# Optimization experiments

Measured on AMD Instinct MI355X. Metric: run time of the kernel, lower is better.

The kernel has to match this reference:

```python
import jax, jax.numpy as jnp
import numpy as np

B, T, D, DS = 8, 4096, 1024, 64


def setup_inputs() -> dict:
    key = jax.random.key(0)
    ks = jax.random.split(key, 9)
    s = 0.02
    return {
        "x": jax.random.normal(ks[0], (B, T, D), dtype=jnp.float32),
        "Wq": jax.random.normal(ks[1], (DS, D), dtype=jnp.float32) * s,
        "bq": jnp.zeros((DS,), dtype=jnp.float32),
        "Wk": jax.random.normal(ks[2], (DS, D), dtype=jnp.float32) * s,
        "bk": jnp.zeros((DS,), dtype=jnp.float32),
        "Wv": jax.random.normal(ks[3], (DS, D), dtype=jnp.float32) * s,
        "bv": jnp.zeros((DS,), dtype=jnp.float32),
        "decay": jnp.full((DS,), 0.95, dtype=jnp.float32),
        "Wo": jax.random.normal(ks[4], (D, DS), dtype=jnp.float32) * s,
        "bo": jnp.zeros((D,), dtype=jnp.float32),
    }


def reference(x, Wq, bq, Wk, bk, Wv, bv, decay, Wo, bo):
    # projections: [B,T,DS]
    q = jnp.einsum('btd,sd->bts', x, Wq) + bq
    k = jnp.einsum('btd,sd->bts', x, Wk) + bk
    v = jnp.einsum('btd,sd->bts', x, Wv) + bv
    d = jax.nn.sigmoid(decay)  # [DS]

    def step(S, qkv_t):
        q_t, k_t, v_t = qkv_t  # each [B, DS]
        # diag(d) @ S + v k^T  (rank-1 update per batch)
        S = d[None, :, None] * S + v_t[:, :, None] * k_t[:, None, :]
        o = jnp.einsum('bij,bj->bi', S, q_t)
        return S, o

    S0 = jnp.zeros((x.shape[0], d.shape[0], d.shape[0]), dtype=x.dtype)
    qkv = (jnp.swapaxes(q, 0, 1), jnp.swapaxes(k, 0, 1), jnp.swapaxes(v, 0, 1))  # [T,B,DS]
    _, outs = jax.lax.scan(step, S0, qkv)  # outs: [T,B,DS]
    scan_out = jnp.swapaxes(outs, 0, 1)  # [B,T,DS]
    return x + jnp.einsum('bts,ds->btd', scan_out, Wo) + bo
```

## Files before the change

kernel.cpp:

```cpp
#include <hip/hip_runtime.h>
#include <cstdint>
#include <cstddef>
#include <cmath>

#define Bb 8
#define Tt 4096
#define Dd 1024
#define DS 64
#define Mm (Bb*Tt)
#define PAD 68

typedef __bf16 bf16x8 __attribute__((ext_vector_type(8)));
typedef __bf16 bf16x4v __attribute__((ext_vector_type(4)));
typedef float f32x4 __attribute__((ext_vector_type(4)));

__device__ __forceinline__ float4* ldsP(float* buf, int row, int col4) {
  return (float4*)(buf + row * PAD + (((col4) ^ ((row >> 3) & 7)) << 2));
}

__global__ __launch_bounds__(256) void convert_w(
    const float* __restrict__ Wq, const float* __restrict__ Wk,
    const float* __restrict__ Wv, const float* __restrict__ Wo,
    __bf16* __restrict__ Wqkvb, __bf16* __restrict__ Wob)
{
  int idx = blockIdx.x * 256 + threadIdx.x;
  if (idx < 196608) {
    float v = (idx < 65536) ? Wq[idx]
            : (idx < 131072) ? Wk[idx - 65536] : Wv[idx - 131072];
    Wqkvb[idx] = (__bf16)v;
  }
  if (idx < 65536) Wob[idx] = (__bf16)Wo[idx];
}

__global__ __launch_bounds__(256) void qkv_mfma(
    const float* __restrict__ x, const __bf16* __restrict__ Wb,
    const float* __restrict__ bq, const float* __restrict__ bk,
    const float* __restrict__ bv, float* __restrict__ qkv)
{
  __shared__ __bf16 xs[2][64 * 64];

  const int tid = threadIdx.x;
  const int w   = tid >> 6;
  const int l   = tid & 63;
  const int m0  = blockIdx.x * 64;
  const int c0  = w * 48;
  const int lr  = l & 15;
  const int lk  = l >> 4;

  const int sr0 = tid >> 4;
  const int sc4 = tid & 15;
  const float* xsrc = x + (size_t)(m0 + sr0) * 1024 + sc4 * 4;

  f32x4 acc[3][4] = {};

  float4 f[4];
  #pragma unroll
  for (int g = 0; g < 4; ++g)
    f[g] = *(const float4*)(xsrc + (size_t)g * 16 * 1024);
  #pragma unroll
  for (int g = 0; g < 4; ++g) {
    bf16x4v h;
    h[0] = (__bf16)f[g].x; h[1] = (__bf16)f[g].y;
    h[2] = (__bf16)f[g].z; h[3] = (__bf16)f[g].w;
    int row = sr0 + 16 * g;
    *(bf16x4v*)((char*)xs[0] + row * 128 + ((sc4 * 8) ^ ((row & 7) << 4))) = h;
  }

  int cur = 0;
  for (int k0 = 0; k0 < 1024; k0 += 64) {
    const bool hasNext = (k0 + 64 < 1024);
    if (hasNext) {
      #pragma unroll
      for (int g = 0; g < 4; ++g)
        f[g] = *(const float4*)(xsrc + (size_t)g * 16 * 1024 + k0 + 64);
    }

    __syncthreads();

    if (hasNext) {
      #pragma unroll
      for (int g = 0; g < 4; ++g) {
        bf16x4v h;
        h[0] = (__bf16)f[g].x; h[1] = (__bf16)f[g].y;
        h[2] = (__bf16)f[g].z; h[3] = (__bf16)f[g].w;
        int row = sr0 + 16 * g;
        *(bf16x4v*)((char*)xs[cur ^ 1] + row * 128 + ((sc4 * 8) ^ ((row & 7) << 4))) = h;
      }
    }

    #pragma unroll
    for (int ks = 0; ks < 2; ++ks) {
      bf16x8 wf[3], xf[4];
      #pragma unroll
      for (int jf = 0; jf < 3; ++jf)
        wf[jf] = *(const bf16x8*)(Wb + (size_t)(c0 + jf * 16 + lr) * 1024
                                     + k0 + ks * 32 + lk * 8);
      #pragma unroll
      for (int mf = 0; mf < 4; ++mf) {
        int row = mf * 16 + lr;
        int boff = row * 128 + ((ks * 64 + lk * 16) ^ ((row & 7) << 4));
        xf[mf] = *(const bf16x8*)((const char*)xs[cur] + boff);
      }
      #pragma unroll
      for (int jf = 0; jf < 3; ++jf)
        #pragma unroll
        for (int mf = 0; mf < 4; ++mf)
          acc[jf][mf] = __builtin_amdgcn_mfma_f32_16x16x32_bf16(
              wf[jf], xf[mf], acc[jf][mf], 0, 0, 0);
    }
    cur ^= 1;
  }

  #pragma unroll
  for (int jf = 0; jf < 3; ++jf) {
    int j0 = c0 + jf * 16 + lk * 4;
    const float* bsrc = (j0 < 64) ? (bq + j0)
                      : (j0 < 128) ? (bk + j0 - 64) : (bv + j0 - 128);
    float4 b4 = *(const float4*)bsrc;
    #pragma unroll
    for (int mf = 0; mf < 4; ++mf) {
      int m = m0 + mf * 16 + lr;
      float4 o;
      o.x = acc[jf][mf][0] + b4.x;
      o.y = acc[jf][mf][1] + b4.y;
      o.z = acc[jf][mf][2] + b4.z;
      o.w = acc[jf][mf][3] + b4.w;
      *(float4*)(qkv + (size_t)m * 192 + j0) = o;
    }
  }
}

__global__ __launch_bounds__(256) void scan_chunk_a(
    const float* __restrict__ qkv, const float* __restrict__ decay,
    float* __restrict__ Ubuf, float* __restrict__ so)
{
  __shared__ float Qs[64 * PAD];
  __shared__ float Ks[64 * PAD];
  __shared__ float Vs[64 * PAD];
  __shared__ float l2d[64];

  const int tid = threadIdx.x;
  const int bc  = blockIdx.x;
  const int b   = bc >> 6;
  const int ch  = bc & 63;
  const int ti  = tid >> 4;
  const int tj  = tid & 15;

  const float* base = qkv + ((size_t)(b * Tt + ch * 64)) * 192;

  #pragma unroll
  for (int it = 0; it < 12; ++it) {
    int idx = tid + it * 256;
    int row = idx / 48, f = idx % 48;
    float4 g = *(const float4*)(base + (size_t)row * 192 + f * 4);
    float4* dst;
    if (f < 16)      dst = ldsP(Qs, row, f);
    else if (f < 32) dst = ldsP(Ks, row, f - 16);
    else             dst = ldsP(Vs, row, f - 32);
    *dst = g;
  }
  if (tid < 64) {
    float d = 1.0f / (1.0f + expf(-decay[tid]));
    l2d[tid] = log2f(d);
  }
  __syncthreads();

  {
    int s = tid >> 2;
    #pragma unroll
    for (int g4 = 0; g4 < 4; ++g4) {
      int col4 = (tid & 3) * 4 + g4;
      float4* p = ldsP(Vs, s, col4);
      float4 v = *p;
      float e0 = exp2f(-(float)s * l2d[col4 * 4 + 0]);
      float e1 = exp2f(-(float)s * l2d[col4 * 4 + 1]);
      float e2 = exp2f(-(float)s * l2d[col4 * 4 + 2]);
      float e3 = exp2f(-(float)s * l2d[col4 * 4 + 3]);
      v.x *= e0; v.y *= e1; v.z *= e2; v.w *= e3;
      *p = v;
    }
  }

  float gval[4][4] = {};
  #pragma unroll
  for (int kk4 = 0; kk4 < 16; ++kk4) {
    float4 K4[4], Q4[4];
    #pragma unroll
    for (int r = 0; r < 4; ++r) K4[r] = *ldsP(Ks, ti * 4 + r, kk4);
    #pragma unroll
    for (int c = 0; c < 4; ++c) Q4[c] = *ldsP(Qs, tj * 4 + c, kk4);
    #pragma unroll
    for (int r = 0; r < 4; ++r)
      #pragma unroll
      for (int c = 0; c < 4; ++c) {
        gval[r][c] = fmaf(K4[r].x, Q4[c].x, gval[r][c]);
        gval[r][c] = fmaf(K4[r].y, Q4[c].y, gval[r][c]);
        gval[r][c] = fmaf(K4[r].z, Q4[c].z, gval[r][c]);
        gval[r][c] = fmaf(K4[r].w, Q4[c].w, gval[r][c]);
      }
  }
  #pragma unroll
  for (int r = 0; r < 4; ++r)
    #pragma unroll
    for (int c = 0; c < 4; ++c)
      if (ti * 4 + r > tj * 4 + c) gval[r][c] = 0.0f;

  __syncthreads();

  #pragma unroll
  for (int r = 0; r < 4; ++r) {
    float4 g4 = {gval[r][0], gval[r][1], gval[r][2], gval[r][3]};
    *ldsP(Qs, ti * 4 + r, tj) = g4;
  }
  __syncthreads();

  float uacc[4][4] = {};
  float oacc[4][4] = {};
  for (int s = 0; s < 64; ++s) {
    float4 Vti = *ldsP(Vs, s, ti);
    float4 Ktj = *ldsP(Ks, s, tj);
    float4 Gti = *ldsP(Qs, s, ti);
    float4 Vtj = *ldsP(Vs, s, tj);
    const float vi[4] = {Vti.x, Vti.y, Vti.z, Vti.w};
    const float kj[4] = {Ktj.x, Ktj.y, Ktj.z, Ktj.w};
    const float gu[4] = {Gti.x, Gti.y, Gti.z, Gti.w};
    const float vj[4] = {Vtj.x, Vtj.y, Vtj.z, Vtj.w};
    #pragma unroll
    for (int r = 0; r < 4; ++r)
      #pragma unroll
      for (int c = 0; c < 4; ++c) {
        uacc[r][c] = fmaf(vi[r], kj[c], uacc[r][c]);
        oacc[r][c] = fmaf(gu[r], vj[c], oacc[r][c]);
      }
  }

  #pragma unroll
  for (int r = 0; r < 4; ++r) {
    int i = ti * 4 + r;
    float d63 = exp2f(63.0f * l2d[i]);
    float4 o = {uacc[r][0] * d63, uacc[r][1] * d63,
                uacc[r][2] * d63, uacc[r][3] * d63};
    *(float4*)(Ubuf + ((size_t)bc * 64 + i) * 64 + tj * 4) = o;
  }
  #pragma unroll
  for (int r = 0; r < 4; ++r) {
    int u = ti * 4 + r;
    float e0 = exp2f((float)u * l2d[tj * 4 + 0]);
    float e1 = exp2f((float)u * l2d[tj * 4 + 1]);
    float e2 = exp2f((float)u * l2d[tj * 4 + 2]);
    float e3 = exp2f((float)u * l2d[tj * 4 + 3]);
    float4 o = {oacc[r][0] * e0, oacc[r][1] * e1,
                oacc[r][2] * e2, oacc[r][3] * e3};
    *(float4*)(so + ((size_t)(b * Tt + ch * 64 + u)) * 64 + tj * 4) = o;
  }
}

__global__ __launch_bounds__(64) void scan_state(
    const float* __restrict__ decay, float* __restrict__ Ubuf)
{
  const int b  = blockIdx.x >> 4;
  const int jq = blockIdx.x & 15;
  const int i  = threadIdx.x;

  float d = 1.0f / (1.0f + expf(-decay[i]));
  float d2 = d * d, d4 = d2 * d2, d8 = d4 * d4;
  float d16 = d8 * d8, d32 = d16 * d16, d64 = d32 * d32;

  float* base = Ubuf + ((size_t)b * 64) * 4096 + (size_t)i * 64 + jq * 4;

  float4 S = {0.f, 0.f, 0.f, 0.f};
  float4 u0 = *(const float4*)(base + 0 * 4096);
  float4 u1 = *(const float4*)(base + 1 * 4096);
  float4 u2 = *(const float4*)(base + 2 * 4096);
  float4 u3 = *(const float4*)(base + 3 * 4096);

  for (int c = 0; c < 64; c += 4) {
    float4 n0 = u0, n1 = u1, n2 = u2, n3 = u3;
    if (c + 4 < 64) {
      n0 = *(const float4*)(base + (size_t)(c + 4) * 4096);
      n1 = *(const float4*)(base + (size_t)(c + 5) * 4096);
      n2 = *(const float4*)(base + (size_t)(c + 6) * 4096);
      n3 = *(const float4*)(base + (size_t)(c + 7) * 4096);
    }
    *(float4*)(base + (size_t)(c + 0) * 4096) = S;
    S.x = fmaf(d64, S.x, u0.x); S.y = fmaf(d64, S.y, u0.y);
    S.z = fmaf(d64, S.z, u0.z); S.w = fmaf(d64, S.w, u0.w);
    *(float4*)(base + (size_t)(c + 1) * 4096) = S;
    S.x = fmaf(d64, S.x, u1.x); S.y = fmaf(d64, S.y, u1.y);
    S.z = fmaf(d64, S.z, u1.z); S.w = fmaf(d64, S.w, u1.w);
    *(float4*)(base + (size_t)(c + 2) * 4096) = S;
    S.x = fmaf(d64, S.x, u2.x); S.y = fmaf(d64, S.y, u2.y);
    S.z = fmaf(d64, S.z, u2.z); S.w = fmaf(d64, S.w, u2.w);
    *(float4*)(base + (size_t)(c + 3) * 4096) = S;
    S.x = fmaf(d64, S.x, u3.x); S.y = fmaf(d64, S.y, u3.y);
    S.z = fmaf(d64, S.z, u3.z); S.w = fmaf(d64, S.w, u3.w);
    u0 = n0; u1 = n1; u2 = n2; u3 = n3;
  }
}

__global__ __launch_bounds__(256) void scan_chunk_c(
    const float* __restrict__ qkv, const float* __restrict__ decay,
    const float* __restrict__ Sbuf, const float* __restrict__ so,
    __bf16* __restrict__ sob)
{
  __shared__ float Ss[64 * PAD];
  __shared__ float Qs[64 * PAD];
  __shared__ float l2d[64];

  const int tid = threadIdx.x;
  const int bc  = blockIdx.x;
  const int b   = bc >> 6;
  const int ch  = bc & 63;
  const int ti  = tid >> 4;
  const int tj  = tid & 15;

  #pragma unroll
  for (int it = 0; it < 4; ++it) {
    int idx = tid + it * 256;
    int row = idx >> 4, col4 = idx & 15;
    float4 s4 = *(const float4*)(Sbuf + (size_t)bc * 4096 + (size_t)row * 64 + col4 * 4);
    *ldsP(Ss, row, col4) = s4;
    float4 q4 = *(const float4*)(qkv + ((size_t)(b * Tt + ch * 64 + row)) * 192 + col4 * 4);
    *ldsP(Qs, row, col4) = q4;
  }
  if (tid < 64) {
    float d = 1.0f / (1.0f + expf(-decay[tid]));
    l2d[tid] = log2f(d);
  }
  __syncthreads();

  float acc[4][4] = {};
  #pragma unroll
  for (int j4 = 0; j4 < 16; ++j4) {
    float4 Q4[4], S4[4];
    #pragma unroll
    for (int r = 0; r < 4; ++r) Q4[r] = *ldsP(Qs, ti * 4 + r, j4);
    #pragma unroll
    for (int c = 0; c < 4; ++c) S4[c] = *ldsP(Ss, tj * 4 + c, j4);
    #pragma unroll
    for (int r = 0; r < 4; ++r)
      #pragma unroll
      for (int c = 0; c < 4; ++c) {
        acc[r][c] = fmaf(Q4[r].x, S4[c].x, acc[r][c]);
        acc[r][c] = fmaf(Q4[r].y, S4[c].y, acc[r][c]);
        acc[r][c] = fmaf(Q4[r].z, S4[c].z, acc[r][c]);
        acc[r][c] = fmaf(Q4[r].w, S4[c].w, acc[r][c]);
      }
  }

  #pragma unroll
  for (int r = 0; r < 4; ++r) {
    int u = ti * 4 + r;
    size_t row = (size_t)(b * Tt + ch * 64 + u);
    float4 prev = *(const float4*)(so + row * 64 + tj * 4);
    float e0 = exp2f((float)(u + 1) * l2d[tj * 4 + 0]);
    float e1 = exp2f((float)(u + 1) * l2d[tj * 4 + 1]);
    float e2 = exp2f((float)(u + 1) * l2d[tj * 4 + 2]);
    float e3 = exp2f((float)(u + 1) * l2d[tj * 4 + 3]);
    bf16x4v ov;
    ov[0] = (__bf16)fmaf(acc[r][0], e0, prev.x);
    ov[1] = (__bf16)fmaf(acc[r][1], e1, prev.y);
    ov[2] = (__bf16)fmaf(acc[r][2], e2, prev.z);
    ov[3] = (__bf16)fmaf(acc[r][3], e3, prev.w);
    *(bf16x4v*)(sob + row * 64 + tj * 4) = ov;
  }
}

__global__ __launch_bounds__(256) void out_mfma(
    const float* __restrict__ x, const __bf16* __restrict__ sob,
    const __bf16* __restrict__ Wob, const float* __restrict__ bo,
    float* __restrict__ out)
{
  __shared__ float ps[4][16 * 64];

  const int bid = blockIdx.x;
  const int rb  = bid >> 2;
  const int jq  = bid & 3;
  const int w   = threadIdx.x >> 6;
  const int l   = threadIdx.x & 63;
  const int lr  = l & 15;
  const int lk  = l >> 4;
  const int m0  = rb * 64 + w * 16;
  const int er  = l >> 4;
  const int ec  = l & 15;

  const __bf16* bp = sob + (size_t)(m0 + lr) * 64 + lk * 8;
  bf16x8 bf0 = *(const bf16x8*)(bp);
  bf16x8 bf1 = *(const bf16x8*)(bp + 32);

  float* myps = ps[w];

  #pragma unroll
  for (int jj = 0; jj < 4; ++jj) {
    const int j0 = (jq * 4 + jj) * 64;

    float4 xv[4];
    #pragma unroll
    for (int k = 0; k < 4; ++k)
      xv[k] = *(const float4*)(x + (size_t)(m0 + er + 4 * k) * 1024 + j0 + ec * 4);
    float4 b4 = *(const float4*)(bo + j0 + ec * 4);

    const __bf16* ap = Wob + (size_t)(j0 + lr) * 64 + lk * 8;
    f32x4 acc[4];
    #pragma unroll
    for (int jf = 0; jf < 4; ++jf) {
      bf16x8 a0 = *(const bf16x8*)(ap + (size_t)jf * 16 * 64);
      bf16x8 a1 = *(const bf16x8*)(ap + (size_t)jf * 16 * 64 + 32);
      f32x4 t = {0.f, 0.f, 0.f, 0.f};
      t = __builtin_amdgcn_mfma_f32_16x16x32_bf16(a0, bf0, t, 0, 0, 0);
      t = __builtin_amdgcn_mfma_f32_16x16x32_bf16(a1, bf1, t, 0, 0, 0);
      acc[jf] = t;
    }

    #pragma unroll
    for (int jf = 0; jf < 4; ++jf) {
      int c4 = jf * 4 + lk;
      float4 v = {acc[jf][0], acc[jf][1], acc[jf][2], acc[jf][3]};
      *(float4*)((char*)myps + lr * 256 + ((c4 * 16) ^ ((lr & 7) << 4))) = v;
    }

    #pragma unroll
    for (int k = 0; k < 4; ++k) {
      int r = er + 4 * k;
      float4 pv = *(const float4*)((char*)myps + r * 256 + ((ec * 16) ^ ((r & 7) << 4)));
      size_t m = (size_t)(m0 + r);
      float4 o;
      o.x = xv[k].x + pv.x + b4.x;
      o.y = xv[k].y + pv.y + b4.y;
      o.z = xv[k].z + pv.z + b4.z;
      o.w = xv[k].w + pv.w + b4.w;
      *(float4*)(out + m * 1024 + j0 + ec * 4) = o;
    }
  }
}

extern "C" void kernel_launch(void* const* d_in, const int* in_sizes, int n_in,
                              void* d_out, int out_size, void* d_ws, size_t ws_size,
                              hipStream_t stream)
{
  const float* x   = (const float*)d_in[0];
  const float* Wq  = (const float*)d_in[1];
  const float* bq  = (const float*)d_in[2];
  const float* Wk  = (const float*)d_in[3];
  const float* bk  = (const float*)d_in[4];
  const float* Wv  = (const float*)d_in[5];
  const float* bv  = (const float*)d_in[6];
  const float* dec = (const float*)d_in[7];
  const float* Wo  = (const float*)d_in[8];
  const float* bo  = (const float*)d_in[9];
  float* out = (float*)d_out;

  float*  qkv   = (float*)d_ws;
  float*  so    = qkv + (size_t)Mm * 192;
  float*  Ubuf  = so + (size_t)Mm * 64;
  __bf16* sob   = (__bf16*)(Ubuf + (size_t)512 * 4096);
  __bf16* Wqkvb = sob + (size_t)Mm * 64;
  __bf16* Wob   = Wqkvb + (size_t)192 * 1024;

  convert_w<<<768, 256, 0, stream>>>(Wq, Wk, Wv, Wo, Wqkvb, Wob);
  qkv_mfma<<<Mm / 64, 256, 0, stream>>>(x, Wqkvb, bq, bk, bv, qkv);
  scan_chunk_a<<<512, 256, 0, stream>>>(qkv, dec, Ubuf, so);
  scan_state<<<128, 64, 0, stream>>>(dec, Ubuf);
  scan_chunk_c<<<512, 256, 0, stream>>>(qkv, dec, Ubuf, so, sob);
  out_mfma<<<2048, 256, 0, stream>>>(x, sob, Wob, bo, out);
}
```

Baseline: 360.1 us.

## Store QKV in bf16, prefetch weights and x, use nontemporal loads/stores

The QKV intermediate is now written as bf16 instead of fp32, which halves its write and read traffic between the projection and both scan kernels. The QKV GEMM register-prefetches the next weight fragments one k-step ahead and reads x with nontemporal loads. The output kernel prefetches the next x tile and bias before the MFMA work and writes results with nontemporal stores. The cost is lower precision in q/k/v feeding the recurrent scan, which may raise numerical error.

```diff
diff --git a/kernel.cpp b/kernel.cpp
--- a/kernel.cpp
+++ b/kernel.cpp
@@ -35,7 +35,7 @@
 __global__ __launch_bounds__(256) void qkv_mfma(
     const float* __restrict__ x, const __bf16* __restrict__ Wb,
     const float* __restrict__ bq, const float* __restrict__ bk,
-    const float* __restrict__ bv, float* __restrict__ qkv)
+    const float* __restrict__ bv, __bf16* __restrict__ qkvb)
 {
   __shared__ __bf16 xs[2][64 * 64];
 
@@ -53,18 +53,23 @@
 
   f32x4 acc[3][4] = {};
 
-  float4 f[4];
+  f32x4 f[4];
   #pragma unroll
   for (int g = 0; g < 4; ++g)
-    f[g] = *(const float4*)(xsrc + (size_t)g * 16 * 1024);
+    f[g] = __builtin_nontemporal_load((const f32x4*)(xsrc + (size_t)g * 16 * 1024));
   #pragma unroll
   for (int g = 0; g < 4; ++g) {
     bf16x4v h;
-    h[0] = (__bf16)f[g].x; h[1] = (__bf16)f[g].y;
-    h[2] = (__bf16)f[g].z; h[3] = (__bf16)f[g].w;
+    h[0] = (__bf16)f[g][0]; h[1] = (__bf16)f[g][1];
+    h[2] = (__bf16)f[g][2]; h[3] = (__bf16)f[g][3];
     int row = sr0 + 16 * g;
     *(bf16x4v*)((char*)xs[0] + row * 128 + ((sc4 * 8) ^ ((row & 7) << 4))) = h;
   }
+
+  const __bf16* wp = Wb + (size_t)(c0 + lr) * 1024 + lk * 8;
+  bf16x8 wc0 = *(const bf16x8*)(wp + 0 * 16 * 1024);
+  bf16x8 wc1 = *(const bf16x8*)(wp + 1 * 16 * 1024);
+  bf16x8 wc2 = *(const bf16x8*)(wp + 2 * 16 * 1024);
 
   int cur = 0;
   for (int k0 = 0; k0 < 1024; k0 += 64) {
@@ -72,7 +77,8 @@
     if (hasNext) {
       #pragma unroll
       for (int g = 0; g < 4; ++g)
-        f[g] = *(const float4*)(xsrc + (size_t)g * 16 * 1024 + k0 + 64);
+        f[g] = __builtin_nontemporal_load(
+            (const f32x4*)(xsrc + (size_t)g * 16 * 1024 + k0 + 64));
     }
 
     __syncthreads();
@@ -81,8 +87,8 @@
       #pragma unroll
       for (int g = 0; g < 4; ++g) {
         bf16x4v h;
-        h[0] = (__bf16)f[g].x; h[1] = (__bf16)f[g].y;
-        h[2] = (__bf16)f[g].z; h[3] = (__bf16)f[g].w;
+        h[0] = (__bf16)f[g][0]; h[1] = (__bf16)f[g][1];
+        h[2] = (__bf16)f[g][2]; h[3] = (__bf16)f[g][3];
         int row = sr0 + 16 * g;
         *(bf16x4v*)((char*)xs[cur ^ 1] + row * 128 + ((sc4 * 8) ^ ((row & 7) << 4))) = h;
       }
@@ -90,11 +96,14 @@
 
     #pragma unroll
     for (int ks = 0; ks < 2; ++ks) {
-      bf16x8 wf[3], xf[4];
-      #pragma unroll
-      for (int jf = 0; jf < 3; ++jf)
-        wf[jf] = *(const bf16x8*)(Wb + (size_t)(c0 + jf * 16 + lr) * 1024
-                                     + k0 + ks * 32 + lk * 8);
+      const int knext = k0 + ks * 32 + 32;
+      bf16x8 wn0, wn1, wn2;
+      if (knext < 1024) {
+        wn0 = *(const bf16x8*)(wp + 0 * 16 * 1024 + knext);
+        wn1 = *(const bf16x8*)(wp + 1 * 16 * 1024 + knext);
+        wn2 = *(const bf16x8*)(wp + 2 * 16 * 1024 + knext);
+      }
+      bf16x8 xf[4];
       #pragma unroll
       for (int mf = 0; mf < 4; ++mf) {
         int row = mf * 16 + lr;
@@ -102,11 +111,12 @@
         xf[mf] = *(const bf16x8*)((const char*)xs[cur] + boff);
       }
       #pragma unroll
-      for (int jf = 0; jf < 3; ++jf)
-        #pragma unroll
-        for (int mf = 0; mf < 4; ++mf)
-          acc[jf][mf] = __builtin_amdgcn_mfma_f32_16x16x32_bf16(
-              wf[jf], xf[mf], acc[jf][mf], 0, 0, 0);
+      for (int mf = 0; mf < 4; ++mf) {
+        acc[0][mf] = __builtin_amdgcn_mfma_f32_16x16x32_bf16(wc0, xf[mf], acc[0][mf], 0, 0, 0);
+        acc[1][mf] = __builtin_amdgcn_mfma_f32_16x16x32_bf16(wc1, xf[mf], acc[1][mf], 0, 0, 0);
+        acc[2][mf] = __builtin_amdgcn_mfma_f32_16x16x32_bf16(wc2, xf[mf], acc[2][mf], 0, 0, 0);
+      }
+      if (knext < 1024) { wc0 = wn0; wc1 = wn1; wc2 = wn2; }
     }
     cur ^= 1;
   }
@@ -120,18 +130,18 @@
     #pragma unroll
     for (int mf = 0; mf < 4; ++mf) {
       int m = m0 + mf * 16 + lr;
-      float4 o;
-      o.x = acc[jf][mf][0] + b4.x;
-      o.y = acc[jf][mf][1] + b4.y;
-      o.z = acc[jf][mf][2] + b4.z;
-      o.w = acc[jf][mf][3] + b4.w;
-      *(float4*)(qkv + (size_t)m * 192 + j0) = o;
+      bf16x4v o;
+      o[0] = (__bf16)(acc[jf][mf][0] + b4.x);
+      o[1] = (__bf16)(acc[jf][mf][1] + b4.y);
+      o[2] = (__bf16)(acc[jf][mf][2] + b4.z);
+      o[3] = (__bf16)(acc[jf][mf][3] + b4.w);
+      *(bf16x4v*)(qkvb + (size_t)m * 192 + j0) = o;
     }
   }
 }
 
 __global__ __launch_bounds__(256) void scan_chunk_a(
-    const float* __restrict__ qkv, const float* __restrict__ decay,
+    const __bf16* __restrict__ qkvb, const float* __restrict__ decay,
     float* __restrict__ Ubuf, float* __restrict__ so)
 {
   __shared__ float Qs[64 * PAD];
@@ -146,18 +156,19 @@
   const int ti  = tid >> 4;
   const int tj  = tid & 15;
 
-  const float* base = qkv + ((size_t)(b * Tt + ch * 64)) * 192;
-
-  #pragma unroll
-  for (int it = 0; it < 12; ++it) {
+  const __bf16* base = qkvb + ((size_t)(b * Tt + ch * 64)) * 192;
+
+  #pragma unroll
+  for (int it = 0; it < 6; ++it) {
     int idx = tid + it * 256;
-    int row = idx / 48, f = idx % 48;
-    float4 g = *(const float4*)(base + (size_t)row * 192 + f * 4);
-    float4* dst;
-    if (f < 16)      dst = ldsP(Qs, row, f);
-    else if (f < 32) dst = ldsP(Ks, row, f - 16);
-    else             dst = ldsP(Vs, row, f - 32);
-    *dst = g;
+    int row = idx / 24, fq = idx % 24;
+    bf16x8 h = *(const bf16x8*)(base + (size_t)row * 192 + fq * 8);
+    float4 lo = {(float)h[0], (float)h[1], (float)h[2], (float)h[3]};
+    float4 hi = {(float)h[4], (float)h[5], (float)h[6], (float)h[7]};
+    int seg = fq >> 3, c2 = (fq & 7) * 2;
+    float* dst = (seg == 0) ? Qs : (seg == 1) ? Ks : Vs;
+    *ldsP(dst, row, c2)     = lo;
+    *ldsP(dst, row, c2 + 1) = hi;
   }
   if (tid < 64) {
     float d = 1.0f / (1.0f + expf(-decay[tid]));
@@ -299,7 +310,7 @@
 }
 
 __global__ __launch_bounds__(256) void scan_chunk_c(
-    const float* __restrict__ qkv, const float* __restrict__ decay,
+    const __bf16* __restrict__ qkvb, const float* __restrict__ decay,
     const float* __restrict__ Sbuf, const float* __restrict__ so,
     __bf16* __restrict__ sob)
 {
@@ -320,8 +331,16 @@
     int row = idx >> 4, col4 = idx & 15;
     float4 s4 = *(const float4*)(Sbuf + (size_t)bc * 4096 + (size_t)row * 64 + col4 * 4);
     *ldsP(Ss, row, col4) = s4;
-    float4 q4 = *(const float4*)(qkv + ((size_t)(b * Tt + ch * 64 + row)) * 192 + col4 * 4);
-    *ldsP(Qs, row, col4) = q4;
+  }
+  #pragma unroll
+  for (int it = 0; it < 2; ++it) {
+    int idx = tid + it * 256;
+    int row = idx >> 3, fq = idx & 7;
+    bf16x8 h = *(const bf16x8*)(qkvb + ((size_t)(b * Tt + ch * 64 + row)) * 192 + fq * 8);
+    float4 lo = {(float)h[0], (float)h[1], (float)h[2], (float)h[3]};
+    float4 hi = {(float)h[4], (float)h[5], (float)h[6], (float)h[7]};
+    *ldsP(Qs, row, fq * 2)     = lo;
+    *ldsP(Qs, row, fq * 2 + 1) = hi;
   }
   if (tid < 64) {
     float d = 1.0f / (1.0f + expf(-decay[tid]));
@@ -385,20 +404,34 @@
   const int ec  = l & 15;
 
   const __bf16* bp = sob + (size_t)(m0 + lr) * 64 + lk * 8;
-  bf16x8 bf0 = *(const bf16x8*)(bp);
-  bf16x8 bf1 = *(const bf16x8*)(bp + 32);
+  bf16x8 bfr0 = *(const bf16x8*)(bp);
+  bf16x8 bfr1 = *(const bf16x8*)(bp + 32);
 
   float* myps = ps[w];
 
+  f32x4 cxv[4]; f32x4 cb4;
+  {
+    const int j0 = jq * 256;
+    #pragma unroll
+    for (int k = 0; k < 4; ++k)
+      cxv[k] = __builtin_nontemporal_load(
+          (const f32x4*)(x + (size_t)(m0 + er + 4 * k) * 1024 + j0 + ec * 4));
+    cb4 = *(const f32x4*)(bo + j0 + ec * 4);
+  }
+
   #pragma unroll
   for (int jj = 0; jj < 4; ++jj) {
-    const int j0 = (jq * 4 + jj) * 64;
-
-    float4 xv[4];
-    #pragma unroll
-    for (int k = 0; k < 4; ++k)
-      xv[k] = *(const float4*)(x + (size_t)(m0 + er + 4 * k) * 1024 + j0 + ec * 4);
-    float4 b4 = *(const float4*)(bo + j0 + ec * 4);
+    const int j0 = jq * 256 + jj * 64;
+
+    f32x4 nxv[4]; f32x4 nb4;
+    if (jj < 3) {
+      const int jn = j0 + 64;
+      #pragma unroll
+      for (int k = 0; k < 4; ++k)
+        nxv[k] = __builtin_nontemporal_load(
+            (const f32x4*)(x + (size_t)(m0 + er + 4 * k) * 1024 + jn + ec * 4));
+      nb4 = *(const f32x4*)(bo + jn + ec * 4);
+    }
 
     const __bf16* ap = Wob + (size_t)(j0 + lr) * 64 + lk * 8;
     f32x4 acc[4];
@@ -407,8 +440,8 @@
       bf16x8 a0 = *(const bf16x8*)(ap + (size_t)jf * 16 * 64);
       bf16x8 a1 = *(const bf16x8*)(ap + (size_t)jf * 16 * 64 + 32);
       f32x4 t = {0.f, 0.f, 0.f, 0.f};
-      t = __builtin_amdgcn_mfma_f32_16x16x32_bf16(a0, bf0, t, 0, 0, 0);
-      t = __builtin_amdgcn_mfma_f32_16x16x32_bf16(a1, bf1, t, 0, 0, 0);
+      t = __builtin_amdgcn_mfma_f32_16x16x32_bf16(a0, bfr0, t, 0, 0, 0);
+      t = __builtin_amdgcn_mfma_f32_16x16x32_bf16(a1, bfr1, t, 0, 0, 0);
       acc[jf] = t;
     }
 
@@ -424,12 +457,18 @@
       int r = er + 4 * k;
       float4 pv = *(const float4*)((char*)myps + r * 256 + ((ec * 16) ^ ((r & 7) << 4)));
       size_t m = (size_t)(m0 + r);
-      float4 o;
-      o.x = xv[k].x + pv.x + b4.x;
-      o.y = xv[k].y + pv.y + b4.y;
-      o.z = xv[k].z + pv.z + b4.z;
-      o.w = xv[k].w + pv.w + b4.w;
-      *(float4*)(out + m * 1024 + j0 + ec * 4) = o;
+      f32x4 o;
+      o[0] = cxv[k][0] + pv.x + cb4[0];
+      o[1] = cxv[k][1] + pv.y + cb4[1];
+      o[2] = cxv[k][2] + pv.z + cb4[2];
+      o[3] = cxv[k][3] + pv.w + cb4[3];
+      __builtin_nontemporal_store(o, (f32x4*)(out + m * 1024 + j0 + ec * 4));
+    }
+
+    if (jj < 3) {
+      #pragma unroll
+      for (int k = 0; k < 4; ++k) cxv[k] = nxv[k];
+      cb4 = nb4;
     }
   }
 }
@@ -450,17 +489,17 @@
   const float* bo  = (const float*)d_in[9];
   float* out = (float*)d_out;
 
-  float*  qkv   = (float*)d_ws;
-  float*  so    = qkv + (size_t)Mm * 192;
+  __bf16* qkvb  = (__bf16*)d_ws;
+  float*  so    = (float*)(qkvb + (size_t)Mm * 192);
   float*  Ubuf  = so + (size_t)Mm * 64;
   __bf16* sob   = (__bf16*)(Ubuf + (size_t)512 * 4096);
   __bf16* Wqkvb = sob + (size_t)Mm * 64;
   __bf16* Wob   = Wqkvb + (size_t)192 * 1024;
 
   convert_w<<<768, 256, 0, stream>>>(Wq, Wk, Wv, Wo, Wqkvb, Wob);
-  qkv_mfma<<<Mm / 64, 256, 0, stream>>>(x, Wqkvb, bq, bk, bv, qkv);
-  scan_chunk_a<<<512, 256, 0, stream>>>(qkv, dec, Ubuf, so);
+  qkv_mfma<<<Mm / 64, 256, 0, stream>>>(x, Wqkvb, bq, bk, bv, qkvb);
+  scan_chunk_a<<<512, 256, 0, stream>>>(qkvb, dec, Ubuf, so);
   scan_state<<<128, 64, 0, stream>>>(dec, Ubuf);
-  scan_chunk_c<<<512, 256, 0, stream>>>(qkv, dec, Ubuf, so, sob);
+  scan_chunk_c<<<512, 256, 0, stream>>>(qkvb, dec, Ubuf, so, sob);
   out_mfma<<<2048, 256, 0, stream>>>(x, sob, Wob, bo, out);
 }
```

After: 348.2 us. 1.03x faster.
